# Kernel tuning notes

Hardware: AMD Instinct MI355X
Metric: run time of the kernel (lower is better)

Reference implementation:

```python
import jax, jax.numpy as jnp
import numpy as np

B, T, V, D, H, C = 256, 512, 400000, 50, 50, 5  # batch, seq, vocab, emb_dim, lstm_hidden, classes


def setup_inputs() -> dict:
    key = jax.random.key(0)
    ks = jax.random.split(key, 9)
    x = jax.random.randint(ks[0], (B, T), 0, V)
    lengths = jax.random.randint(ks[1], (B,), 1, T + 1)
    bows = jnp.zeros((B, 1), dtype=jnp.float32)  # unused by the model
    emb_table = jax.random.normal(ks[2], (V, D), dtype=jnp.float32) * 0.1
    s = 1.0 / np.sqrt(H)
    W_ih = jax.random.uniform(ks[3], (4 * H, D), minval=-s, maxval=s, dtype=jnp.float32)
    W_hh = jax.random.uniform(ks[4], (4 * H, H), minval=-s, maxval=s, dtype=jnp.float32)
    b_ih = jax.random.uniform(ks[5], (4 * H,), minval=-s, maxval=s, dtype=jnp.float32)
    b_hh = jax.random.uniform(ks[6], (4 * H,), minval=-s, maxval=s, dtype=jnp.float32)
    sl = 1.0 / np.sqrt(3 * H)
    W_lin = jax.random.uniform(ks[7], (C, 3 * H), minval=-sl, maxval=sl, dtype=jnp.float32)
    b_lin = jax.random.uniform(ks[8], (C,), minval=-sl, maxval=sl, dtype=jnp.float32)
    return {"x": x, "lengths": lengths, "bows": bows, "emb_table": emb_table,
            "W_ih": W_ih, "W_hh": W_hh, "b_ih": b_ih, "b_hh": b_hh,
            "W_lin": W_lin, "b_lin": b_lin}


def _lstm(emb, W_ih, W_hh, b_ih, b_hh):
    # emb: [B,T,D] -> h_all: [B,T,H]; PyTorch gate order i,f,g,o
    xp = jnp.einsum('btd,gd->btg', emb, W_ih) + b_ih + b_hh  # [B,T,4H]
    xp_t = jnp.swapaxes(xp, 0, 1)  # [T,B,4H]
    h0 = jnp.zeros((emb.shape[0], W_hh.shape[1]), emb.dtype)
    c0 = jnp.zeros_like(h0)

    def step(carry, xt):
        h, c = carry
        g = xt + h @ W_hh.T
        i, f, gg, o = jnp.split(g, 4, axis=-1)
        i, f, o = jax.nn.sigmoid(i), jax.nn.sigmoid(f), jax.nn.sigmoid(o)
        c = f * c + i * jnp.tanh(gg)
        h = o * jnp.tanh(c)
        return (h, c), h

    _, h_all = jax.lax.scan(step, (h0, c0), xp_t)
    return jnp.swapaxes(h_all, 0, 1)  # [B,T,H]


def reference(x, lengths, bows, emb_table, W_ih, W_hh, b_ih, b_hh, W_lin, b_lin):
    emb = emb_table[x]                              # [B,T,D]
    h_all = _lstm(emb, W_ih, W_hh, b_ih, b_hh)      # [B,T,H]
    idx = jnp.minimum(lengths, h_all.shape[1]) - 1  # last valid timestep
    last = jnp.take_along_axis(h_all, idx[:, None, None], axis=1)[:, 0, :]  # [B,H]
    # faithful to original: sum over full padded seq / length, max over full padded seq
    mean = jnp.sum(emb, axis=1) / lengths[:, None].astype(emb.dtype)        # [B,D]
    mx = jnp.max(emb, axis=1)                                               # [B,D]
    rep = jnp.concatenate([last, mean, mx], axis=1)                          # [B,3H]
    return rep @ W_lin.T + b_lin
```

## Files before the change

kernel.cpp:

```cpp
#include <hip/hip_runtime.h>
#include <cmath>

#define NB 256
#define NT 512
#define ND 50
#define NH 50
#define NC 5

typedef float f32x4 __attribute__((ext_vector_type(4)));
typedef float f32x2 __attribute__((ext_vector_type(2)));

__device__ __forceinline__ float rcpf(float x) { return __builtin_amdgcn_rcpf(x); }
__device__ __forceinline__ float rdl(float v, int l) {
    return __int_as_float(__builtin_amdgcn_readlane(__float_as_int(v), l));
}
__device__ __forceinline__ void gload4(f32x4& d, const float* p) {
    asm volatile("global_load_dwordx4 %0, %1, off" : "=v"(d) : "v"(p));
}

#define FENCE_BAR                                             \
    asm volatile("s_waitcnt lgkmcnt(0)" ::: "memory");        \
    __builtin_amdgcn_s_barrier();                             \
    asm volatile("" ::: "memory");

__global__ __launch_bounds__(256)
void k0_prep(const float* __restrict__ W_hh, const float* __restrict__ W_ih,
             float* __restrict__ wsWih, float* __restrict__ wsWhh)
{
    int idx = blockIdx.x * 256 + threadIdx.x;
    if (idx < 200 * 52) {
        int d = idx / 52, c = idx - (idx / 52) * 52;
        wsWih[idx] = (c < ND) ? W_ih[d * ND + c] : 0.f;
    } else if (idx < 2 * 200 * 52) {
        int j = idx - 200 * 52;
        int d = j / 52, c = j - (j / 52) * 52;
        wsWhh[j] = (c < NH) ? W_hh[d * NH + c] : 0.f;
    }
}

#define DECLROW(P) f32x4 P##_0{},P##_1{},P##_2{},P##_3{},P##_4{},P##_5{},P##_6{},P##_7{}, \
                         P##_8{},P##_9{},P##_10{},P##_11{},P##_12{};
#define LOADROW(P,B) { const float* b_=(B); \
    gload4(P##_0,b_+0);  gload4(P##_1,b_+4);  gload4(P##_2,b_+8);  gload4(P##_3,b_+12); \
    gload4(P##_4,b_+16); gload4(P##_5,b_+20); gload4(P##_6,b_+24); gload4(P##_7,b_+28); \
    gload4(P##_8,b_+32); gload4(P##_9,b_+36); gload4(P##_10,b_+40); gload4(P##_11,b_+44); \
    gload4(P##_12,b_+48); }

#define DOTI(J, HP) { f32x4 h4 = (HP)[J];                          \
    a0 = fmaf(h4.x, w##J.x, a0); a1 = fmaf(h4.y, w##J.y, a1);     \
    a2 = fmaf(h4.z, w##J.z, a2); a3 = fmaf(h4.w, w##J.w, a3); }
#define DOTI13(HP) DOTI(0,HP) DOTI(1,HP) DOTI(2,HP) DOTI(3,HP) DOTI(4,HP) DOTI(5,HP) \
    DOTI(6,HP) DOTI(7,HP) DOTI(8,HP) DOTI(9,HP) DOTI(10,HP) DOTI(11,HP) DOTI(12,HP)

__global__ __launch_bounds__(256)
void k1_xproj(const int* __restrict__ x, const int* __restrict__ lengths,
              const float* __restrict__ emb_table,
              const float* __restrict__ wsWih, const float* __restrict__ b_ih,
              const float* __restrict__ b_hh,
              float* __restrict__ xp, int t0, int t1, int tiles, int tcAlloc)
{
    const int b    = blockIdx.x / tiles;
    const int tile = blockIdx.x % tiles;
    const int rt0  = t0 + tile * 64;
    if (rt0 >= t1) return;
    if (rt0 >= lengths[b]) return;
    const int nrows = min(64, t1 - rt0);

    __shared__ int xv[64];
    __shared__ __align__(16) float eL[64][52];

    const int tid = threadIdx.x;

    float bsum = 0.f;
    const float* wrow = wsWih + tid * 52;
    f32x4 w0{},w1{},w2{},w3{},w4{},w5{},w6{},w7{},w8{},w9{},w10{},w11{},w12{};
    gload4(w0,wrow+0); gload4(w1,wrow+4); gload4(w2,wrow+8); gload4(w3,wrow+12);
    gload4(w4,wrow+16); gload4(w5,wrow+20); gload4(w6,wrow+24); gload4(w7,wrow+28);
    gload4(w8,wrow+32); gload4(w9,wrow+36); gload4(w10,wrow+40); gload4(w11,wrow+44);
    gload4(w12,wrow+48);
    if (tid < 200) bsum = b_ih[tid] + b_hh[tid];
    if (tid < nrows) xv[tid] = x[(size_t)b * NT + rt0 + tid];
    __syncthreads();
    for (int idx = tid; idx < nrows * 52; idx += 256) {
        int row = idx / 52, col = idx - row * 52;
        eL[row][col] = (col < ND) ? emb_table[(size_t)xv[row] * ND + col] : 0.f;
    }
    asm volatile("s_waitcnt vmcnt(0)" ::: "memory");
    __builtin_amdgcn_sched_barrier(0);
    __syncthreads();
    if (tid < 200) {
        const int wr = 4 * (tid % NH) + (tid / NH);
        float* xpb = xp + ((size_t)b * tcAlloc + (rt0 - t0)) * 200 + wr;
        for (int row = 0; row < nrows; ++row) {
            const f32x4* ep = (const f32x4*)&eL[row][0];
            float a0 = bsum, a1 = 0.f, a2 = 0.f, a3 = 0.f;
            DOTI13(ep)
            xpb[(size_t)row * 200] = (a0 + a1) + (a2 + a3);
        }
    }
}

#define FMA2(H,W,A) __builtin_elementwise_fma((H),(W),(A))
#define CDOT1(SEED,OUT) { f32x2 A01 = {(SEED), 0.f}, A23 = {0.f, 0.f};        \
    A01=FMA2(hp0 ,CW_0.xy ,A01); A23=FMA2(hp1 ,CW_0.zw ,A23);                 \
    A01=FMA2(hp2 ,CW_1.xy ,A01); A23=FMA2(hp3 ,CW_1.zw ,A23);                 \
    A01=FMA2(hp4 ,CW_2.xy ,A01); A23=FMA2(hp5 ,CW_2.zw ,A23);                 \
    A01=FMA2(hp6 ,CW_3.xy ,A01); A23=FMA2(hp7 ,CW_3.zw ,A23);                 \
    A01=FMA2(hp8 ,CW_4.xy ,A01); A23=FMA2(hp9 ,CW_4.zw ,A23);                 \
    A01=FMA2(hp10,CW_5.xy ,A01); A23=FMA2(hp11,CW_5.zw ,A23);                 \
    A01=FMA2(hp12,CW_6.xy ,A01); A23=FMA2(hp13,CW_6.zw ,A23);                 \
    A01=FMA2(hp14,CW_7.xy ,A01); A23=FMA2(hp15,CW_7.zw ,A23);                 \
    A01=FMA2(hp16,CW_8.xy ,A01); A23=FMA2(hp17,CW_8.zw ,A23);                 \
    A01=FMA2(hp18,CW_9.xy ,A01); A23=FMA2(hp19,CW_9.zw ,A23);                 \
    A01=FMA2(hp20,CW_10.xy,A01); A23=FMA2(hp21,CW_10.zw,A23);                 \
    A01=FMA2(hp22,CW_11.xy,A01); A23=FMA2(hp23,CW_11.zw,A23);                 \
    A23=FMA2(hp24,CW_12.xy,A23);                                              \
    OUT = (A01.x + A01.y) + (A23.x + A23.y); }

#define SSTEP(XQ, S) {                                                        \
    f32x2 hp0 ={rdl(hv,0 ),rdl(hv,1 )}, hp1 ={rdl(hv,2 ),rdl(hv,3 )};         \
    f32x2 hp2 ={rdl(hv,4 ),rdl(hv,5 )}, hp3 ={rdl(hv,6 ),rdl(hv,7 )};         \
    f32x2 hp4 ={rdl(hv,8 ),rdl(hv,9 )}, hp5 ={rdl(hv,10),rdl(hv,11)};         \
    f32x2 hp6 ={rdl(hv,12),rdl(hv,13)}, hp7 ={rdl(hv,14),rdl(hv,15)};         \
    f32x2 hp8 ={rdl(hv,16),rdl(hv,17)}, hp9 ={rdl(hv,18),rdl(hv,19)};         \
    f32x2 hp10={rdl(hv,20),rdl(hv,21)}, hp11={rdl(hv,22),rdl(hv,23)};         \
    f32x2 hp12={rdl(hv,24),rdl(hv,25)}, hp13={rdl(hv,26),rdl(hv,27)};         \
    f32x2 hp14={rdl(hv,28),rdl(hv,29)}, hp15={rdl(hv,30),rdl(hv,31)};         \
    f32x2 hp16={rdl(hv,32),rdl(hv,33)}, hp17={rdl(hv,34),rdl(hv,35)};         \
    f32x2 hp18={rdl(hv,36),rdl(hv,37)}, hp19={rdl(hv,38),rdl(hv,39)};         \
    f32x2 hp20={rdl(hv,40),rdl(hv,41)}, hp21={rdl(hv,42),rdl(hv,43)};         \
    f32x2 hp22={rdl(hv,44),rdl(hv,45)}, hp23={rdl(hv,46),rdl(hv,47)};         \
    f32x2 hp24={rdl(hv,48),rdl(hv,49)};                                       \
    float gg;                                                                 \
    CDOT1(XQ, gg)                                                             \
    { int sn_ = (S) + 4; if (sn_ > nsteps - 1) sn_ = nsteps - 1;              \
      XQ = xpb[(size_t)sn_ * 200]; }                                          \
    float act = fmaf(rcpf(1.f + __expf(-sce * gg)), sce, ade);                \
    abuf[(S) & 1][wid][kln] = act;                                            \
    FENCE_BAR                                                                 \
    float i_ = abuf[(S) & 1][0][kln];                                         \
    float f_ = abuf[(S) & 1][1][kln];                                         \
    float gt = abuf[(S) & 1][2][kln];                                         \
    float o_ = abuf[(S) & 1][3][kln];                                         \
    cst = fmaf(f_, cst, i_ * gt);                                             \
    float th = fmaf(rcpf(1.f + __expf(-2.f * cst)), 2.f, -1.f);               \
    hv = o_ * th;                                                             \
    hkeep = (t0 + (S) == lastidx) ? hv : hkeep;                               \
}

__global__ __launch_bounds__(256)
__attribute__((amdgpu_waves_per_eu(1, 1)))
void k2_scan(const int* __restrict__ lengths, const float* __restrict__ wsWhh,
             const float* __restrict__ xp,
             float* __restrict__ stH, float* __restrict__ stC, float* __restrict__ lastH,
             int t0, int t1, int tcAlloc)
{
    const int b   = blockIdx.x, tid = threadIdx.x;
    const int wid = tid >> 6;
    const int kln = tid & 63;
    const int kc  = (kln < NH) ? kln : NH - 1;

    __shared__ __align__(16) float abuf[2][4][64];

    const int lastidx = min(lengths[b], NT) - 1;
    const int nsteps  = t1 - t0;

    float hv  = (t0 == 0) ? 0.f : stH[b * NH + kc];
    float cst = (t0 == 0) ? 0.f : stC[b * NH + kc];

    DECLROW(CW)
    LOADROW(CW, wsWhh + ((size_t)wid * NH + kc) * 52)
    asm volatile("s_waitcnt vmcnt(0)" ::: "memory");
    __builtin_amdgcn_sched_barrier(0);

    const float sce = (wid == 2) ? 2.f : 1.f;
    const float ade = (wid == 2) ? -1.f : 0.f;

    const float* xpb = xp + (size_t)b * tcAlloc * 200 + 4 * kc + wid;
    float xq0 = xpb[0];
    float xq1 = xpb[200];
    float xq2 = xpb[400];
    float xq3 = xpb[600];
    float hkeep = 0.f;

    for (int s4 = 0; s4 < nsteps; s4 += 4) {
        SSTEP(xq0, s4 + 0)
        SSTEP(xq1, s4 + 1)
        SSTEP(xq2, s4 + 2)
        SSTEP(xq3, s4 + 3)
    }

    if (wid == 0 && kln < NH) {
        stH[b * NH + kln] = hv;
        stC[b * NH + kln] = cst;
        if (lastidx >= t0 && lastidx < t1) lastH[b * NH + kln] = hkeep;
    }
}

__global__ __launch_bounds__(256)
void k3_final(const int* __restrict__ x, const int* __restrict__ lengths,
              const float* __restrict__ emb_table,
              const float* __restrict__ W_lin, const float* __restrict__ b_lin,
              const float* __restrict__ lastH, float* __restrict__ out)
{
    const int b = blockIdx.x, tid = threadIdx.x;
    __shared__ int xv[NT];
    __shared__ float ps[5][52], pm[5][52];
    __shared__ float rep[160];

    for (int i = tid; i < NT; i += 256) xv[i] = x[(size_t)b * NT + i];
    __syncthreads();
    const int g = tid / ND, d = tid - g * ND;
    if (tid < 250) {
        float s = 0.f, m = -INFINITY;
        #pragma unroll 4
        for (int t = g; t < NT; t += 5) {
            float e = emb_table[(size_t)xv[t] * ND + d];
            s += e; m = fmaxf(m, e);
        }
        ps[g][d] = s; pm[g][d] = m;
    }
    __syncthreads();
    if (tid < NH) {
        float s = ps[0][tid] + ps[1][tid] + ps[2][tid] + ps[3][tid] + ps[4][tid];
        float m = fmaxf(fmaxf(fmaxf(pm[0][tid], pm[1][tid]), fmaxf(pm[2][tid], pm[3][tid])), pm[4][tid]);
        rep[tid]          = lastH[b * NH + tid];
        rep[NH + tid]     = s / (float)lengths[b];
        rep[2 * NH + tid] = m;
    }
    __syncthreads();
    if (tid < NC) {
        float acc = b_lin[tid];
        #pragma unroll 5
        for (int j = 0; j < 3 * NH; ++j)
            acc = fmaf(rep[j], W_lin[tid * 3 * NH + j], acc);
        out[(size_t)b * NC + tid] = acc;
    }
}

extern "C" void kernel_launch(void* const* d_in, const int* in_sizes, int n_in,
                              void* d_out, int out_size, void* d_ws, size_t ws_size,
                              hipStream_t stream) {
    const int*   x     = (const int*)d_in[0];
    const int*   len   = (const int*)d_in[1];
    const float* emb   = (const float*)d_in[3];
    const float* W_ih  = (const float*)d_in[4];
    const float* W_hh  = (const float*)d_in[5];
    const float* b_ih  = (const float*)d_in[6];
    const float* b_hh  = (const float*)d_in[7];
    const float* W_lin = (const float*)d_in[8];
    const float* b_lin = (const float*)d_in[9];
    float* outp = (float*)d_out;

    float* stH   = (float*)d_ws;
    float* stC   = stH + NB * NH;
    float* lastH = stC + NB * NH;
    float* wsWih = (float*)((char*)d_ws + 160 * 1024);
    float* wsWhh = wsWih + 200 * 52;
    const size_t xpOff = 256 * 1024;
    float* xp = (float*)((char*)d_ws + xpOff);

    size_t avail = (ws_size > xpOff + 8192) ? ws_size - xpOff - 8192 : 0;
    int tc = (int)(avail / ((size_t)NB * 200 * sizeof(float)));
    tc &= ~3;
    if (tc > NT) tc = NT;
    if (tc < 4)  tc = 4;

    hipLaunchKernelGGL(k0_prep, dim3(82), dim3(256), 0, stream, W_hh, W_ih, wsWih, wsWhh);

    for (int t0 = 0; t0 < NT; t0 += tc) {
        const int t1 = min(NT, t0 + tc);
        const int tiles = (t1 - t0 + 63) / 64;
        hipLaunchKernelGGL(k1_xproj, dim3(NB * tiles), dim3(256), 0, stream,
                           x, len, emb, wsWih, b_ih, b_hh, xp, t0, t1, tiles, tc);
        hipLaunchKernelGGL(k2_scan, dim3(NB), dim3(256), 0, stream,
                           len, wsWhh, xp, stH, stC, lastH, t0, t1, tc);
    }
    hipLaunchKernelGGL(k3_final, dim3(NB), dim3(256), 0, stream,
                       x, len, emb, W_lin, b_lin, lastH, outp);
}
```

Before: 268.9 us.

## Fuse input projection into LSTM scan with producer waves and LDS ring

The separate input-projection kernel, which wrote a full per-timestep gate preactivation array to global memory, is removed. The scan kernel now runs 512 threads: four waves do the recurrence while four producer waves gather embeddings and compute the input projection 8 steps ahead into a 16-slot shared-memory ring. Both roles share the per-step barrier. This drops the large global write/read round trip and the chunked multi-launch loop. In exchange, producer waves share SIMDs and barriers with the latency-critical scan. Projection is also now computed for every timestep, with no early exit past each sequence length.

```diff
diff --git a/kernel.cpp b/kernel.cpp
--- a/kernel.cpp
+++ b/kernel.cpp
@@ -45,60 +45,6 @@
     gload4(P##_4,b_+16); gload4(P##_5,b_+20); gload4(P##_6,b_+24); gload4(P##_7,b_+28); \
     gload4(P##_8,b_+32); gload4(P##_9,b_+36); gload4(P##_10,b_+40); gload4(P##_11,b_+44); \
     gload4(P##_12,b_+48); }
-
-#define DOTI(J, HP) { f32x4 h4 = (HP)[J];                          \
-    a0 = fmaf(h4.x, w##J.x, a0); a1 = fmaf(h4.y, w##J.y, a1);     \
-    a2 = fmaf(h4.z, w##J.z, a2); a3 = fmaf(h4.w, w##J.w, a3); }
-#define DOTI13(HP) DOTI(0,HP) DOTI(1,HP) DOTI(2,HP) DOTI(3,HP) DOTI(4,HP) DOTI(5,HP) \
-    DOTI(6,HP) DOTI(7,HP) DOTI(8,HP) DOTI(9,HP) DOTI(10,HP) DOTI(11,HP) DOTI(12,HP)
-
-__global__ __launch_bounds__(256)
-void k1_xproj(const int* __restrict__ x, const int* __restrict__ lengths,
-              const float* __restrict__ emb_table,
-              const float* __restrict__ wsWih, const float* __restrict__ b_ih,
-              const float* __restrict__ b_hh,
-              float* __restrict__ xp, int t0, int t1, int tiles, int tcAlloc)
-{
-    const int b    = blockIdx.x / tiles;
-    const int tile = blockIdx.x % tiles;
-    const int rt0  = t0 + tile * 64;
-    if (rt0 >= t1) return;
-    if (rt0 >= lengths[b]) return;
-    const int nrows = min(64, t1 - rt0);
-
-    __shared__ int xv[64];
-    __shared__ __align__(16) float eL[64][52];
-
-    const int tid = threadIdx.x;
-
-    float bsum = 0.f;
-    const float* wrow = wsWih + tid * 52;
-    f32x4 w0{},w1{},w2{},w3{},w4{},w5{},w6{},w7{},w8{},w9{},w10{},w11{},w12{};
-    gload4(w0,wrow+0); gload4(w1,wrow+4); gload4(w2,wrow+8); gload4(w3,wrow+12);
-    gload4(w4,wrow+16); gload4(w5,wrow+20); gload4(w6,wrow+24); gload4(w7,wrow+28);
-    gload4(w8,wrow+32); gload4(w9,wrow+36); gload4(w10,wrow+40); gload4(w11,wrow+44);
-    gload4(w12,wrow+48);
-    if (tid < 200) bsum = b_ih[tid] + b_hh[tid];
-    if (tid < nrows) xv[tid] = x[(size_t)b * NT + rt0 + tid];
-    __syncthreads();
-    for (int idx = tid; idx < nrows * 52; idx += 256) {
-        int row = idx / 52, col = idx - row * 52;
-        eL[row][col] = (col < ND) ? emb_table[(size_t)xv[row] * ND + col] : 0.f;
-    }
-    asm volatile("s_waitcnt vmcnt(0)" ::: "memory");
-    __builtin_amdgcn_sched_barrier(0);
-    __syncthreads();
-    if (tid < 200) {
-        const int wr = 4 * (tid % NH) + (tid / NH);
-        float* xpb = xp + ((size_t)b * tcAlloc + (rt0 - t0)) * 200 + wr;
-        for (int row = 0; row < nrows; ++row) {
-            const f32x4* ep = (const f32x4*)&eL[row][0];
-            float a0 = bsum, a1 = 0.f, a2 = 0.f, a3 = 0.f;
-            DOTI13(ep)
-            xpb[(size_t)row * 200] = (a0 + a1) + (a2 + a3);
-        }
-    }
-}
 
 #define FMA2(H,W,A) __builtin_elementwise_fma((H),(W),(A))
 #define CDOT1(SEED,OUT) { f32x2 A01 = {(SEED), 0.f}, A23 = {0.f, 0.f};        \
@@ -117,84 +63,114 @@
     A23=FMA2(hp24,CW_12.xy,A23);                                              \
     OUT = (A01.x + A01.y) + (A23.x + A23.y); }
 
-#define SSTEP(XQ, S) {                                                        \
-    f32x2 hp0 ={rdl(hv,0 ),rdl(hv,1 )}, hp1 ={rdl(hv,2 ),rdl(hv,3 )};         \
-    f32x2 hp2 ={rdl(hv,4 ),rdl(hv,5 )}, hp3 ={rdl(hv,6 ),rdl(hv,7 )};         \
-    f32x2 hp4 ={rdl(hv,8 ),rdl(hv,9 )}, hp5 ={rdl(hv,10),rdl(hv,11)};         \
-    f32x2 hp6 ={rdl(hv,12),rdl(hv,13)}, hp7 ={rdl(hv,14),rdl(hv,15)};         \
-    f32x2 hp8 ={rdl(hv,16),rdl(hv,17)}, hp9 ={rdl(hv,18),rdl(hv,19)};         \
-    f32x2 hp10={rdl(hv,20),rdl(hv,21)}, hp11={rdl(hv,22),rdl(hv,23)};         \
-    f32x2 hp12={rdl(hv,24),rdl(hv,25)}, hp13={rdl(hv,26),rdl(hv,27)};         \
-    f32x2 hp14={rdl(hv,28),rdl(hv,29)}, hp15={rdl(hv,30),rdl(hv,31)};         \
-    f32x2 hp16={rdl(hv,32),rdl(hv,33)}, hp17={rdl(hv,34),rdl(hv,35)};         \
-    f32x2 hp18={rdl(hv,36),rdl(hv,37)}, hp19={rdl(hv,38),rdl(hv,39)};         \
-    f32x2 hp20={rdl(hv,40),rdl(hv,41)}, hp21={rdl(hv,42),rdl(hv,43)};         \
-    f32x2 hp22={rdl(hv,44),rdl(hv,45)}, hp23={rdl(hv,46),rdl(hv,47)};         \
-    f32x2 hp24={rdl(hv,48),rdl(hv,49)};                                       \
-    float gg;                                                                 \
-    CDOT1(XQ, gg)                                                             \
-    { int sn_ = (S) + 4; if (sn_ > nsteps - 1) sn_ = nsteps - 1;              \
-      XQ = xpb[(size_t)sn_ * 200]; }                                          \
-    float act = fmaf(rcpf(1.f + __expf(-sce * gg)), sce, ade);                \
-    abuf[(S) & 1][wid][kln] = act;                                            \
+#define PT(J,EV) a0=fmaf(rdl(EV,4*J+0),CW_##J.x,a0); a1=fmaf(rdl(EV,4*J+1),CW_##J.y,a1); \
+                 a2=fmaf(rdl(EV,4*J+2),CW_##J.z,a2); a3=fmaf(rdl(EV,4*J+3),CW_##J.w,a3);
+#define PRODROW(EV,SLOT) { float a0=bq,a1=0.f,a2=0.f,a3=0.f;                  \
+    PT(0,EV) PT(1,EV) PT(2,EV) PT(3,EV) PT(4,EV) PT(5,EV) PT(6,EV)            \
+    PT(7,EV) PT(8,EV) PT(9,EV) PT(10,EV) PT(11,EV) PT(12,EV)                  \
+    float xpv = (a0 + a1) + (a2 + a3);                                        \
+    if (kln < NH) ring[(SLOT) & 15][pw][kln] = xpv; }
+
+#define STEPF(EI, S) {                                                        \
+    if (isScan) {                                                             \
+        float xq = ring[(S) & 15][wid][kln];                                  \
+        f32x2 hp0 ={rdl(hv,0 ),rdl(hv,1 )}, hp1 ={rdl(hv,2 ),rdl(hv,3 )};     \
+        f32x2 hp2 ={rdl(hv,4 ),rdl(hv,5 )}, hp3 ={rdl(hv,6 ),rdl(hv,7 )};     \
+        f32x2 hp4 ={rdl(hv,8 ),rdl(hv,9 )}, hp5 ={rdl(hv,10),rdl(hv,11)};     \
+        f32x2 hp6 ={rdl(hv,12),rdl(hv,13)}, hp7 ={rdl(hv,14),rdl(hv,15)};     \
+        f32x2 hp8 ={rdl(hv,16),rdl(hv,17)}, hp9 ={rdl(hv,18),rdl(hv,19)};     \
+        f32x2 hp10={rdl(hv,20),rdl(hv,21)}, hp11={rdl(hv,22),rdl(hv,23)};     \
+        f32x2 hp12={rdl(hv,24),rdl(hv,25)}, hp13={rdl(hv,26),rdl(hv,27)};     \
+        f32x2 hp14={rdl(hv,28),rdl(hv,29)}, hp15={rdl(hv,30),rdl(hv,31)};     \
+        f32x2 hp16={rdl(hv,32),rdl(hv,33)}, hp17={rdl(hv,34),rdl(hv,35)};     \
+        f32x2 hp18={rdl(hv,36),rdl(hv,37)}, hp19={rdl(hv,38),rdl(hv,39)};     \
+        f32x2 hp20={rdl(hv,40),rdl(hv,41)}, hp21={rdl(hv,42),rdl(hv,43)};     \
+        f32x2 hp22={rdl(hv,44),rdl(hv,45)}, hp23={rdl(hv,46),rdl(hv,47)};     \
+        f32x2 hp24={rdl(hv,48),rdl(hv,49)};                                   \
+        float gg;                                                             \
+        CDOT1(xq, gg)                                                         \
+        float act = fmaf(rcpf(1.f + __expf(-sce * gg)), sce, ade);            \
+        abuf[(S) & 1][wid][kln] = act;                                        \
+    } else if ((S) + 8 < NT) {                                                \
+        PRODROW(EI, (S) + 8)                                                  \
+        int tN = (S) + 12; if (tN > NT - 1) tN = NT - 1;                      \
+        EI = (kln < NH) ? emb_table[(size_t)xls[tN] * ND + kln] : 0.f;        \
+    }                                                                         \
     FENCE_BAR                                                                 \
-    float i_ = abuf[(S) & 1][0][kln];                                         \
-    float f_ = abuf[(S) & 1][1][kln];                                         \
-    float gt = abuf[(S) & 1][2][kln];                                         \
-    float o_ = abuf[(S) & 1][3][kln];                                         \
-    cst = fmaf(f_, cst, i_ * gt);                                             \
-    float th = fmaf(rcpf(1.f + __expf(-2.f * cst)), 2.f, -1.f);               \
-    hv = o_ * th;                                                             \
-    hkeep = (t0 + (S) == lastidx) ? hv : hkeep;                               \
-}
-
-__global__ __launch_bounds__(256)
-__attribute__((amdgpu_waves_per_eu(1, 1)))
-void k2_scan(const int* __restrict__ lengths, const float* __restrict__ wsWhh,
-             const float* __restrict__ xp,
-             float* __restrict__ stH, float* __restrict__ stC, float* __restrict__ lastH,
-             int t0, int t1, int tcAlloc)
+    if (isScan) {                                                             \
+        float i_ = abuf[(S) & 1][0][kln];                                     \
+        float f_ = abuf[(S) & 1][1][kln];                                     \
+        float gt = abuf[(S) & 1][2][kln];                                     \
+        float o_ = abuf[(S) & 1][3][kln];                                     \
+        cst = fmaf(f_, cst, i_ * gt);                                         \
+        float th = fmaf(rcpf(1.f + __expf(-2.f * cst)), 2.f, -1.f);           \
+        hv = o_ * th;                                                         \
+        hkeep = ((S) == lastidx) ? hv : hkeep;                                \
+    }                                                                         \
+}
+
+__global__ __launch_bounds__(512)
+__attribute__((amdgpu_waves_per_eu(2, 2)))
+void k2_fused(const int* __restrict__ x, const int* __restrict__ lengths,
+              const float* __restrict__ emb_table,
+              const float* __restrict__ wsWih, const float* __restrict__ wsWhh,
+              const float* __restrict__ b_ih, const float* __restrict__ b_hh,
+              float* __restrict__ lastH)
 {
     const int b   = blockIdx.x, tid = threadIdx.x;
     const int wid = tid >> 6;
     const int kln = tid & 63;
     const int kc  = (kln < NH) ? kln : NH - 1;
-
+    const bool isScan = wid < 4;
+    const int  pw  = wid & 3;
+
+    __shared__ __align__(16) float ring[16][4][64];
     __shared__ __align__(16) float abuf[2][4][64];
+    __shared__ int xls[NT];
+
+    xls[tid] = x[(size_t)b * NT + tid];
+    __syncthreads();
 
     const int lastidx = min(lengths[b], NT) - 1;
-    const int nsteps  = t1 - t0;
-
-    float hv  = (t0 == 0) ? 0.f : stH[b * NH + kc];
-    float cst = (t0 == 0) ? 0.f : stC[b * NH + kc];
-
+
+    const float* wrow = isScan ? (wsWhh + ((size_t)wid * NH + kc) * 52)
+                               : (wsWih + ((size_t)pw  * NH + kc) * 52);
     DECLROW(CW)
-    LOADROW(CW, wsWhh + ((size_t)wid * NH + kc) * 52)
+    LOADROW(CW, wrow)
+    float bq = 0.f;
+    if (!isScan) bq = b_ih[pw * NH + kc] + b_hh[pw * NH + kc];
     asm volatile("s_waitcnt vmcnt(0)" ::: "memory");
     __builtin_amdgcn_sched_barrier(0);
 
     const float sce = (wid == 2) ? 2.f : 1.f;
     const float ade = (wid == 2) ? -1.f : 0.f;
 
-    const float* xpb = xp + (size_t)b * tcAlloc * 200 + 4 * kc + wid;
-    float xq0 = xpb[0];
-    float xq1 = xpb[200];
-    float xq2 = xpb[400];
-    float xq3 = xpb[600];
-    float hkeep = 0.f;
-
-    for (int s4 = 0; s4 < nsteps; s4 += 4) {
-        SSTEP(xq0, s4 + 0)
-        SSTEP(xq1, s4 + 1)
-        SSTEP(xq2, s4 + 2)
-        SSTEP(xq3, s4 + 3)
-    }
-
-    if (wid == 0 && kln < NH) {
-        stH[b * NH + kln] = hv;
-        stC[b * NH + kln] = cst;
-        if (lastidx >= t0 && lastidx < t1) lastH[b * NH + kln] = hkeep;
-    }
+    float hv = 0.f, cst = 0.f, hkeep = 0.f;
+
+    for (int p = 0; p < 8; ++p) {
+        if (!isScan) {
+            int xt = xls[p];
+            float ev = (kln < NH) ? emb_table[(size_t)xt * ND + kln] : 0.f;
+            PRODROW(ev, p)
+        }
+        FENCE_BAR
+    }
+    float e0 = 0.f, e1 = 0.f, e2 = 0.f, e3 = 0.f;
+    if (!isScan && kln < NH) {
+        e0 = emb_table[(size_t)xls[8]  * ND + kln];
+        e1 = emb_table[(size_t)xls[9]  * ND + kln];
+        e2 = emb_table[(size_t)xls[10] * ND + kln];
+        e3 = emb_table[(size_t)xls[11] * ND + kln];
+    }
+
+    for (int s4 = 0; s4 < NT; s4 += 4) {
+        STEPF(e0, s4 + 0)
+        STEPF(e1, s4 + 1)
+        STEPF(e2, s4 + 2)
+        STEPF(e3, s4 + 3)
+    }
+
+    if (wid == 0 && kln < NH) lastH[b * NH + kln] = hkeep;
 }
 
 __global__ __launch_bounds__(256)
@@ -252,30 +228,13 @@
     const float* b_lin = (const float*)d_in[9];
     float* outp = (float*)d_out;
 
-    float* stH   = (float*)d_ws;
-    float* stC   = stH + NB * NH;
-    float* lastH = stC + NB * NH;
-    float* wsWih = (float*)((char*)d_ws + 160 * 1024);
+    float* lastH = (float*)d_ws;
+    float* wsWih = (float*)((char*)d_ws + 64 * 1024);
     float* wsWhh = wsWih + 200 * 52;
-    const size_t xpOff = 256 * 1024;
-    float* xp = (float*)((char*)d_ws + xpOff);
-
-    size_t avail = (ws_size > xpOff + 8192) ? ws_size - xpOff - 8192 : 0;
-    int tc = (int)(avail / ((size_t)NB * 200 * sizeof(float)));
-    tc &= ~3;
-    if (tc > NT) tc = NT;
-    if (tc < 4)  tc = 4;
 
     hipLaunchKernelGGL(k0_prep, dim3(82), dim3(256), 0, stream, W_hh, W_ih, wsWih, wsWhh);
-
-    for (int t0 = 0; t0 < NT; t0 += tc) {
-        const int t1 = min(NT, t0 + tc);
-        const int tiles = (t1 - t0 + 63) / 64;
-        hipLaunchKernelGGL(k1_xproj, dim3(NB * tiles), dim3(256), 0, stream,
-                           x, len, emb, wsWih, b_ih, b_hh, xp, t0, t1, tiles, tc);
-        hipLaunchKernelGGL(k2_scan, dim3(NB), dim3(256), 0, stream,
-                           len, wsWhh, xp, stH, stC, lastH, t0, t1, tc);
-    }
+    hipLaunchKernelGGL(k2_fused, dim3(NB), dim3(512), 0, stream,
+                       x, len, emb, wsWih, wsWhh, b_ih, b_hh, lastH);
     hipLaunchKernelGGL(k3_final, dim3(NB), dim3(256), 0, stream,
                        x, len, emb, W_lin, b_lin, lastH, outp);
 }
```

After: 309.0 us. 14.9% more time.

## Compute two LSTM gates per wave in scan kernel, halving block to two waves

Applied to the files above, without the earlier changes.

The recurrent scan kernel now runs 2 waves per block instead of 4. Each wave computes two gate rows: wave 0 handles i and f, wave 1 handles g and o. Each lane holds two weight rows and loads x-projection pairs as float2. This halves the number of waves taking part in the per-step barrier and LDS exchange, which should cut synchronisation latency on the serial critical path. In exchange, each lane does twice the FMA work per step and holds twice the registers.

```diff
diff --git a/kernel.cpp b/kernel.cpp
--- a/kernel.cpp
+++ b/kernel.cpp
@@ -101,20 +101,20 @@
 }
 
 #define FMA2(H,W,A) __builtin_elementwise_fma((H),(W),(A))
-#define CDOT1(SEED,OUT) { f32x2 A01 = {(SEED), 0.f}, A23 = {0.f, 0.f};        \
-    A01=FMA2(hp0 ,CW_0.xy ,A01); A23=FMA2(hp1 ,CW_0.zw ,A23);                 \
-    A01=FMA2(hp2 ,CW_1.xy ,A01); A23=FMA2(hp3 ,CW_1.zw ,A23);                 \
-    A01=FMA2(hp4 ,CW_2.xy ,A01); A23=FMA2(hp5 ,CW_2.zw ,A23);                 \
-    A01=FMA2(hp6 ,CW_3.xy ,A01); A23=FMA2(hp7 ,CW_3.zw ,A23);                 \
-    A01=FMA2(hp8 ,CW_4.xy ,A01); A23=FMA2(hp9 ,CW_4.zw ,A23);                 \
-    A01=FMA2(hp10,CW_5.xy ,A01); A23=FMA2(hp11,CW_5.zw ,A23);                 \
-    A01=FMA2(hp12,CW_6.xy ,A01); A23=FMA2(hp13,CW_6.zw ,A23);                 \
-    A01=FMA2(hp14,CW_7.xy ,A01); A23=FMA2(hp15,CW_7.zw ,A23);                 \
-    A01=FMA2(hp16,CW_8.xy ,A01); A23=FMA2(hp17,CW_8.zw ,A23);                 \
-    A01=FMA2(hp18,CW_9.xy ,A01); A23=FMA2(hp19,CW_9.zw ,A23);                 \
-    A01=FMA2(hp20,CW_10.xy,A01); A23=FMA2(hp21,CW_10.zw,A23);                 \
-    A01=FMA2(hp22,CW_11.xy,A01); A23=FMA2(hp23,CW_11.zw,A23);                 \
-    A23=FMA2(hp24,CW_12.xy,A23);                                              \
+#define CDOTP(P,SEED,OUT) { f32x2 A01 = {(SEED), 0.f}, A23 = {0.f, 0.f};      \
+    A01=FMA2(hp0 ,P##_0.xy ,A01); A23=FMA2(hp1 ,P##_0.zw ,A23);               \
+    A01=FMA2(hp2 ,P##_1.xy ,A01); A23=FMA2(hp3 ,P##_1.zw ,A23);               \
+    A01=FMA2(hp4 ,P##_2.xy ,A01); A23=FMA2(hp5 ,P##_2.zw ,A23);               \
+    A01=FMA2(hp6 ,P##_3.xy ,A01); A23=FMA2(hp7 ,P##_3.zw ,A23);               \
+    A01=FMA2(hp8 ,P##_4.xy ,A01); A23=FMA2(hp9 ,P##_4.zw ,A23);               \
+    A01=FMA2(hp10,P##_5.xy ,A01); A23=FMA2(hp11,P##_5.zw ,A23);               \
+    A01=FMA2(hp12,P##_6.xy ,A01); A23=FMA2(hp13,P##_6.zw ,A23);               \
+    A01=FMA2(hp14,P##_7.xy ,A01); A23=FMA2(hp15,P##_7.zw ,A23);               \
+    A01=FMA2(hp16,P##_8.xy ,A01); A23=FMA2(hp17,P##_8.zw ,A23);               \
+    A01=FMA2(hp18,P##_9.xy ,A01); A23=FMA2(hp19,P##_9.zw ,A23);               \
+    A01=FMA2(hp20,P##_10.xy,A01); A23=FMA2(hp21,P##_10.zw,A23);               \
+    A01=FMA2(hp22,P##_11.xy,A01); A23=FMA2(hp23,P##_11.zw,A23);               \
+    A23=FMA2(hp24,P##_12.xy,A23);                                             \
     OUT = (A01.x + A01.y) + (A23.x + A23.y); }
 
 #define SSTEP(XQ, S) {                                                        \
@@ -131,24 +131,24 @@
     f32x2 hp20={rdl(hv,40),rdl(hv,41)}, hp21={rdl(hv,42),rdl(hv,43)};         \
     f32x2 hp22={rdl(hv,44),rdl(hv,45)}, hp23={rdl(hv,46),rdl(hv,47)};         \
     f32x2 hp24={rdl(hv,48),rdl(hv,49)};                                       \
-    float gg;                                                                 \
-    CDOT1(XQ, gg)                                                             \
+    float gA, gB;                                                             \
+    CDOTP(WA, XQ.x, gA)                                                       \
+    CDOTP(WB, XQ.y, gB)                                                       \
     { int sn_ = (S) + 4; if (sn_ > nsteps - 1) sn_ = nsteps - 1;              \
-      XQ = xpb[(size_t)sn_ * 200]; }                                          \
-    float act = fmaf(rcpf(1.f + __expf(-sce * gg)), sce, ade);                \
-    abuf[(S) & 1][wid][kln] = act;                                            \
+      XQ = *(const f32x2*)&xpb[(size_t)sn_ * 200]; }                          \
+    float actA = fmaf(rcpf(1.f + __expf(-sce * gA)), sce, ade);               \
+    float actB = fmaf(rcpf(1.f + __expf(-gB)), 1.f, 0.f);                     \
+    abuf[(S) & 1][wid][kln] = (f32x2){actA, actB};                            \
     FENCE_BAR                                                                 \
-    float i_ = abuf[(S) & 1][0][kln];                                         \
-    float f_ = abuf[(S) & 1][1][kln];                                         \
-    float gt = abuf[(S) & 1][2][kln];                                         \
-    float o_ = abuf[(S) & 1][3][kln];                                         \
-    cst = fmaf(f_, cst, i_ * gt);                                             \
+    f32x2 if_ = abuf[(S) & 1][0][kln];                            \
+    f32x2 go_ = abuf[(S) & 1][1][kln];                            \
+    cst = fmaf(if_.y, cst, if_.x * go_.x);                                    \
     float th = fmaf(rcpf(1.f + __expf(-2.f * cst)), 2.f, -1.f);               \
-    hv = o_ * th;                                                             \
+    hv = go_.y * th;                                                          \
     hkeep = (t0 + (S) == lastidx) ? hv : hkeep;                               \
 }
 
-__global__ __launch_bounds__(256)
+__global__ __launch_bounds__(128)
 __attribute__((amdgpu_waves_per_eu(1, 1)))
 void k2_scan(const int* __restrict__ lengths, const float* __restrict__ wsWhh,
              const float* __restrict__ xp,
@@ -160,7 +160,7 @@
     const int kln = tid & 63;
     const int kc  = (kln < NH) ? kln : NH - 1;
 
-    __shared__ __align__(16) float abuf[2][4][64];
+    __shared__ __align__(16) f32x2 abuf[2][2][64];
 
     const int lastidx = min(lengths[b], NT) - 1;
     const int nsteps  = t1 - t0;
@@ -168,19 +168,20 @@
     float hv  = (t0 == 0) ? 0.f : stH[b * NH + kc];
     float cst = (t0 == 0) ? 0.f : stC[b * NH + kc];
 
-    DECLROW(CW)
-    LOADROW(CW, wsWhh + ((size_t)wid * NH + kc) * 52)
+    DECLROW(WA) DECLROW(WB)
+    LOADROW(WA, wsWhh + ((size_t)(2 * wid + 0) * NH + kc) * 52)
+    LOADROW(WB, wsWhh + ((size_t)(2 * wid + 1) * NH + kc) * 52)
     asm volatile("s_waitcnt vmcnt(0)" ::: "memory");
     __builtin_amdgcn_sched_barrier(0);
 
-    const float sce = (wid == 2) ? 2.f : 1.f;
-    const float ade = (wid == 2) ? -1.f : 0.f;
-
-    const float* xpb = xp + (size_t)b * tcAlloc * 200 + 4 * kc + wid;
-    float xq0 = xpb[0];
-    float xq1 = xpb[200];
-    float xq2 = xpb[400];
-    float xq3 = xpb[600];
+    const float sce = (wid == 1) ? 2.f : 1.f;
+    const float ade = (wid == 1) ? -1.f : 0.f;
+
+    const float* xpb = xp + (size_t)b * tcAlloc * 200 + 4 * kc + 2 * wid;
+    f32x2 xq0 = *(const f32x2*)&xpb[0];
+    f32x2 xq1 = *(const f32x2*)&xpb[200];
+    f32x2 xq2 = *(const f32x2*)&xpb[400];
+    f32x2 xq3 = *(const f32x2*)&xpb[600];
     float hkeep = 0.f;
 
     for (int s4 = 0; s4 < nsteps; s4 += 4) {
@@ -273,7 +274,7 @@
         const int tiles = (t1 - t0 + 63) / 64;
         hipLaunchKernelGGL(k1_xproj, dim3(NB * tiles), dim3(256), 0, stream,
                            x, len, emb, wsWih, b_ih, b_hh, xp, t0, t1, tiles, tc);
-        hipLaunchKernelGGL(k2_scan, dim3(NB), dim3(256), 0, stream,
+        hipLaunchKernelGGL(k2_scan, dim3(NB), dim3(128), 0, stream,
                            len, wsWhh, xp, stH, stC, lastH, t0, t1, tc);
     }
     hipLaunchKernelGGL(k3_final, dim3(NB), dim3(256), 0, stream,
```

Result: slower. 300.6 us (+11.8%).
